# Kernel optimization log

Measured on AMD Instinct MI355X. Metric: run time of the kernel, lower is better.

The kernel has to match this reference:

```python
import jax, jax.numpy as jnp
import numpy as np

B, T, C, H = 2, 2048, 1024, 16
D = C // H  # head dim


def setup_inputs() -> dict:
    key = jax.random.key(0)
    k1, k2, k3 = jax.random.split(key, 3)
    x = jax.random.normal(k1, (B, T, C), dtype=jnp.float32)
    w_qkv = jax.random.normal(k2, (3 * C, C), dtype=jnp.float32) * (1.0 / np.sqrt(C))
    b_qkv = jnp.zeros((3 * C,), dtype=jnp.float32)
    w_proj = jax.random.normal(k3, (C, C), dtype=jnp.float32) * (1.0 / np.sqrt(C))
    b_proj = jnp.zeros((C,), dtype=jnp.float32)
    return {"x": x, "w_qkv": w_qkv, "b_qkv": b_qkv, "w_proj": w_proj, "b_proj": b_proj}


def reference(x, w_qkv, b_qkv, w_proj, b_proj):
    # torch Linear: y = x @ W^T + b
    qkv = jnp.einsum('btc,oc->bto', x, w_qkv) + b_qkv  # [B,T,3C]
    q, k, v = jnp.split(qkv, 3, axis=-1)
    # [B,T,C] -> [B,H,T,D]
    reshape = lambda t: t.reshape(B, T, H, D).transpose(0, 2, 1, 3)
    q, k, v = reshape(q), reshape(k), reshape(v)
    scale = 1.0 / jnp.sqrt(jnp.float32(C))  # NOTE: full C, as in source
    att = jnp.einsum('bhtd,bhsd->bhts', q, k) * scale  # [B,H,T,T]
    causal = jnp.tril(jnp.ones((T, T), dtype=bool))
    att = jnp.where(causal, att, -jnp.inf)
    att = jax.nn.softmax(att, axis=-1)
    y = jnp.einsum('bhts,bhsd->bhtd', att, v)  # [B,H,T,D]
    y = y.transpose(0, 2, 1, 3).reshape(B, T, C)
    return jnp.einsum('btc,oc->bto', y, w_proj) + b_proj
```

## Files before the change

### kernel.cpp

```cpp
#include <hip/hip_runtime.h>

#define DEVINL __device__ __forceinline__

typedef __attribute__((ext_vector_type(8))) short short8;
typedef __attribute__((ext_vector_type(4))) float f32x4;

DEVINL unsigned f2bf_u(float x) {
  union { float f; unsigned u; } v; v.f = x;
  unsigned r = v.u + 0x7FFF + ((v.u >> 16) & 1);
  return r >> 16;
}
DEVINL unsigned short f2bf(float x) { return (unsigned short)f2bf_u(x); }

DEVINL unsigned cvt_pk_bf16(float lo, float hi) {
  unsigned r;
  asm("v_cvt_pk_bf16_f32 %0, %1, %2" : "=v"(r) : "v"(lo), "v"(hi));
  return r;
}

DEVINL void permlane32_swap(unsigned& a, unsigned& b) {
  asm volatile("v_permlane32_swap_b32 %0, %1" : "+v"(a), "+v"(b));
}
DEVINL void permlane16_swap(unsigned& a, unsigned& b) {
  asm volatile("v_permlane16_swap_b32 %0, %1" : "+v"(a), "+v"(b));
}

#if __has_builtin(__builtin_amdgcn_exp2f)
#define EXP2(x) __builtin_amdgcn_exp2f(x)
#else
#define EXP2(x) exp2f(x)
#endif

DEVINL void gload_lds16(const void* g, void* l) {
  __builtin_amdgcn_global_load_lds(
      (const __attribute__((address_space(1))) unsigned int*)g,
      (__attribute__((address_space(3))) unsigned int*)l, 16, 0, 0);
}

DEVINL short8 as_s8(uint4 v) { union { uint4 u; short8 s; } c; c.u = v; return c.s; }
DEVINL f32x4 fzero() { f32x4 z = {0.f, 0.f, 0.f, 0.f}; return z; }

__global__ __launch_bounds__(256) void cvt3_kernel(
    const float4* __restrict__ x, const float4* __restrict__ wq,
    const float4* __restrict__ wp, ushort4* __restrict__ xo,
    ushort4* __restrict__ wqo, ushort4* __restrict__ wpo) {
  const int N1 = 1048576, N2 = 1835008, NT = 2097152;
  int i = blockIdx.x * blockDim.x + threadIdx.x;
  int stride = gridDim.x * blockDim.x;
  for (; i < NT; i += stride) {
    const float4* s; ushort4* d; int j;
    if (i < N1) { s = x; d = xo; j = i; }
    else if (i < N2) { s = wq; d = wqo; j = i - N1; }
    else { s = wp; d = wpo; j = i - N2; }
    float4 v = s[j];
    ushort4 o;
    o.x = f2bf(v.x); o.y = f2bf(v.y); o.z = f2bf(v.z); o.w = f2bf(v.w);
    d[j] = o;
  }
}

template <int RX, int RY>
__global__ __launch_bounds__(256, 3) void gemm_qkv(
    const ushort* __restrict__ A, const ushort* __restrict__ Bw,
    const float* __restrict__ bias,
    ushort* __restrict__ Qb, ushort* __restrict__ Kb, ushort* __restrict__ Vt,
    int M, int N, int K) {
  __shared__ __align__(16) char smem[32768];
  char* ldsA = smem;
  char* ldsB = smem + 16384;

  int gx = gridDim.x;
  int id = blockIdx.y * gx + blockIdx.x;
  int xcd = id & 7, slot = id >> 3;
  int rw = gx / RX, rh = gridDim.y / RY;
  int bx = (xcd % RX) * rw + slot % rw;
  int by = (xcd / RX) * rh + slot / rw;

  int m0 = by * 128, n0 = bx * 128;
  int t = threadIdx.x;
  int lane = t & 63, w = t >> 6;
  int q = lane & 15, g = lane >> 4;
  int wr = w >> 1, wc = w & 1;

  int Lrow[4], Lcol[4];
#pragma unroll
  for (int i = 0; i < 4; ++i) {
    int L = i * 4096 + t * 16;
    int row = L >> 7, c = L & 127;
    Lrow[i] = row;
    Lcol[i] = c ^ ((row & 7) << 4);
  }
  const char* Abase = (const char*)A + (size_t)m0 * K * 2;
  const char* Bbase = (const char*)Bw + (size_t)n0 * K * 2;

  f32x4 acc[4][4];
#pragma unroll
  for (int i = 0; i < 4; ++i)
#pragma unroll
    for (int j = 0; j < 4; ++j) acc[i][j] = fzero();

  for (int k0 = 0; k0 < K; k0 += 64) {
    __syncthreads();
#pragma unroll
    for (int i = 0; i < 4; ++i) {
      int L = i * 4096 + t * 16;
      gload_lds16(Abase + (size_t)Lrow[i] * (K * 2) + k0 * 2 + Lcol[i], ldsA + L);
    }
#pragma unroll
    for (int i = 0; i < 4; ++i) {
      int L = i * 4096 + t * 16;
      gload_lds16(Bbase + (size_t)Lrow[i] * (K * 2) + k0 * 2 + Lcol[i], ldsB + L);
    }
    __syncthreads();

    uint4 bf[2][4];
#pragma unroll
    for (int s = 0; s < 2; ++s)
#pragma unroll
      for (int nt = 0; nt < 4; ++nt) {
        int row = wc * 64 + nt * 16 + q;
        int addr = row * 128 + ((g * 16 + 64 * s) ^ ((row & 7) << 4));
        bf[s][nt] = *(const uint4*)(ldsB + addr);
      }
#pragma unroll
    for (int mt = 0; mt < 4; ++mt) {
      int row = wr * 64 + mt * 16 + q;
      int a0 = row * 128 + ((g * 16) ^ ((row & 7) << 4));
      int a1 = row * 128 + ((g * 16 + 64) ^ ((row & 7) << 4));
      uint4 af0 = *(const uint4*)(ldsA + a0);
      uint4 af1 = *(const uint4*)(ldsA + a1);
#pragma unroll
      for (int nt = 0; nt < 4; ++nt) {
        acc[mt][nt] = __builtin_amdgcn_mfma_f32_16x16x32_bf16(
            as_s8(af0), as_s8(bf[0][nt]), acc[mt][nt], 0, 0, 0);
        acc[mt][nt] = __builtin_amdgcn_mfma_f32_16x16x32_bf16(
            as_s8(af1), as_s8(bf[1][nt]), acc[mt][nt], 0, 0, 0);
      }
    }
  }

  int mrow0 = m0 + wr * 64;
  int b = mrow0 >> 11, tt0 = mrow0 & 2047;
  if (n0 >= 2048) {
    int hs = (n0 + wc * 64) >> 6;
    int h = hs & 15;
    ushort* vb = Vt + ((size_t)(b * 16 + h) * 64) * 2048;
#pragma unroll
    for (int nt = 0; nt < 4; ++nt) {
      int d = nt * 16 + q;
      float bv = bias[n0 + wc * 64 + nt * 16 + q];
#pragma unroll
      for (int mt = 0; mt < 4; ++mt) {
        uint2 o;
        o.x = cvt_pk_bf16(acc[mt][nt][0] + bv, acc[mt][nt][1] + bv);
        o.y = cvt_pk_bf16(acc[mt][nt][2] + bv, acc[mt][nt][3] + bv);
        *(uint2*)(vb + (size_t)d * 2048 + tt0 + mt * 16 + g * 4) = o;
      }
    }
  } else {
    __syncthreads();
    char* tile = smem + w * 8192;
    float bv[4];
#pragma unroll
    for (int nt = 0; nt < 4; ++nt) bv[nt] = bias[n0 + wc * 64 + nt * 16 + q];
#pragma unroll
    for (int mt = 0; mt < 4; ++mt)
#pragma unroll
      for (int nt = 0; nt < 4; ++nt)
#pragma unroll
        for (int r = 0; r < 4; ++r) {
          int row = mt * 16 + g * 4 + r;
          int bcol = ((nt * 16 + q) * 2) ^ ((row & 7) << 4);
          *(ushort*)(tile + row * 128 + bcol) = f2bf(acc[mt][nt][r] + bv[nt]);
        }
    int hs = (n0 + wc * 64) >> 6;
    int which = hs >> 4, h = hs & 15;
    ushort* dst = which == 0 ? Qb : Kb;
    ushort* dbase = dst + (size_t)(b * 16 + h) * 131072 + (size_t)tt0 * 64;
#pragma unroll
    for (int p = 0; p < 8; ++p) {
      int row = p * 8 + (lane >> 3);
      int bcol = ((lane & 7) * 16) ^ ((row & 7) << 4);
      uint4 v = *(const uint4*)(tile + row * 128 + bcol);
      *(uint4*)(dbase + (size_t)row * 64 + (lane & 7) * 8) = v;
    }
  }
}

__global__ __launch_bounds__(256, 2) void gemm_proj(
    const ushort* __restrict__ A, const ushort* __restrict__ Bw,
    const float* __restrict__ bias, float* __restrict__ Out,
    int M, int N, int K) {
  __shared__ __align__(16) char smem[24576];

  int gx = gridDim.x;
  int id = blockIdx.y * gx + blockIdx.x;
  int xcd = id & 7, slot = id >> 3;
  int bx = slot & 7;
  int by = xcd * 8 + (slot >> 3);

  int m0 = by * 64, n0 = bx * 128;
  int t = threadIdx.x;
  int lane = t & 63, w = t >> 6;
  int q = lane & 15, g = lane >> 4;
  int wr = w >> 1, wc = w & 1;

  int Lrow[4], Lcol[4];
#pragma unroll
  for (int i = 0; i < 4; ++i) {
    int L = i * 4096 + t * 16;
    int row = L >> 7, c = L & 127;
    Lrow[i] = row;
    Lcol[i] = c ^ ((row & 7) << 4);
  }
  const char* Abase = (const char*)A + (size_t)m0 * K * 2;
  const char* Bbase = (const char*)Bw + (size_t)n0 * K * 2;

  f32x4 acc[2][4];
#pragma unroll
  for (int i = 0; i < 2; ++i)
#pragma unroll
    for (int j = 0; j < 4; ++j) acc[i][j] = fzero();

  for (int k0 = 0; k0 < K; k0 += 64) {
    __syncthreads();
#pragma unroll
    for (int i = 0; i < 2; ++i) {
      int L = i * 4096 + t * 16;
      gload_lds16(Abase + (size_t)Lrow[i] * (K * 2) + k0 * 2 + Lcol[i], smem + L);
    }
#pragma unroll
    for (int i = 0; i < 4; ++i) {
      int L = i * 4096 + t * 16;
      gload_lds16(Bbase + (size_t)Lrow[i] * (K * 2) + k0 * 2 + Lcol[i],
                  smem + 8192 + L);
    }
    __syncthreads();

    uint4 bf[2][4];
#pragma unroll
    for (int s = 0; s < 2; ++s)
#pragma unroll
      for (int nt = 0; nt < 4; ++nt) {
        int row = wc * 64 + nt * 16 + q;
        int addr = 8192 + row * 128 + ((g * 16 + 64 * s) ^ ((row & 7) << 4));
        bf[s][nt] = *(const uint4*)(smem + addr);
      }
    __builtin_amdgcn_s_setprio(1);
#pragma unroll
    for (int mt = 0; mt < 2; ++mt) {
      int row = wr * 32 + mt * 16 + q;
      int a0 = row * 128 + ((g * 16) ^ ((row & 7) << 4));
      int a1 = row * 128 + ((g * 16 + 64) ^ ((row & 7) << 4));
      uint4 af0 = *(const uint4*)(smem + a0);
      uint4 af1 = *(const uint4*)(smem + a1);
#pragma unroll
      for (int nt = 0; nt < 4; ++nt) {
        acc[mt][nt] = __builtin_amdgcn_mfma_f32_16x16x32_bf16(
            as_s8(af0), as_s8(bf[0][nt]), acc[mt][nt], 0, 0, 0);
        acc[mt][nt] = __builtin_amdgcn_mfma_f32_16x16x32_bf16(
            as_s8(af1), as_s8(bf[1][nt]), acc[mt][nt], 0, 0, 0);
      }
    }
    __builtin_amdgcn_s_setprio(0);
  }

#pragma unroll
  for (int nt = 0; nt < 4; ++nt) {
    int ncol = n0 + wc * 64 + nt * 16 + q;
    float bv = bias[ncol];
#pragma unroll
    for (int mt = 0; mt < 2; ++mt)
#pragma unroll
      for (int r = 0; r < 4; ++r) {
        int m = m0 + wr * 32 + mt * 16 + g * 4 + r;
        Out[(size_t)m * N + ncol] = acc[mt][nt][r] + bv;
      }
  }
}

__global__ __launch_bounds__(512) void attn_kernel(
    const ushort* __restrict__ Q, const ushort* __restrict__ K,
    const ushort* __restrict__ Vt, ushort* __restrict__ Y) {
  __shared__ __align__(16) char smem[33280];
  const float C44 = 0.0450842298f;
  int id = blockIdx.x;
  int xcd = id & 7, slot = id >> 3;
  int bh = xcd * 4 + (slot & 3);
  int qt = 31 - (slot >> 2);
  int t = threadIdx.x;
  int lane = t & 63, w = t >> 6;
  int q = lane & 15, g = lane >> 4;
  int wq = w & 3, half = w >> 2;
  int b = bh >> 4, hh = bh & 15;

  const char* Kc0 = (const char*)(K + (size_t)bh * 2048 * 64);
  const char* Vc0 = (const char*)(Vt + (size_t)bh * 64 * 2048);

  int tb = t * 16;
  int srow = tb >> 7;
  int scol = (tb & 127) ^ ((srow & 7) << 4);

  int offK[2][2], offV[4];
#pragma unroll
  for (int sub = 0; sub < 2; ++sub)
#pragma unroll
    for (int s = 0; s < 2; ++s) {
      int row = half * 32 + sub * 16 + q;
      offK[sub][s] = row * 128 + ((g * 16 + 64 * s) ^ ((row & 7) << 4));
    }
#pragma unroll
  for (int ds = 0; ds < 4; ++ds) {
    int row = ds * 16 + q;
    offV[ds] = 8192 + row * 128 + ((half * 64 + g * 16) ^ ((row & 7) << 4));
  }

  int nch = qt + 1;
  int qrow0 = qt * 64 + wq * 16;
  int qg = qrow0 + q;

  uint4 qf[2];
  {
    const ushort* Qrow = Q + ((size_t)bh * 2048 + qrow0 + q) * 64;
    qf[0] = *(const uint4*)(Qrow + g * 8);
    qf[1] = *(const uint4*)(Qrow + 32 + g * 8);
  }

  f32x4 oacc[4];
#pragma unroll
  for (int i = 0; i < 4; ++i) oacc[i] = fzero();
  float l_run = 0.f;

  gload_lds16(Kc0 + (size_t)srow * 128 + scol, smem + tb);
  gload_lds16(Vc0 + (size_t)srow * 4096 + scol, smem + 8192 + tb);
  __syncthreads();

  int cur = 0;
#pragma unroll 1
  for (int c = 0; c < nch; ++c) {
    int kv0 = c * 64;
    if (c + 1 < nch) {
      int kn = kv0 + 64;
      char* dstb = smem + (cur ^ 1) * 16384;
      gload_lds16(Kc0 + (size_t)(kn + srow) * 128 + scol, dstb + tb);
      gload_lds16(Vc0 + (size_t)srow * 4096 + (size_t)kn * 2 + scol,
                  dstb + 8192 + tb);
    }
    const char* base = smem + cur * 16384;
    int kst = kv0 + half * 32;
    if (kst <= qrow0 + 15) {
      f32x4 sacc[2];
      __builtin_amdgcn_s_setprio(1);
#pragma unroll
      for (int sub = 0; sub < 2; ++sub) {
        sacc[sub] = fzero();
#pragma unroll
        for (int s = 0; s < 2; ++s)
          sacc[sub] = __builtin_amdgcn_mfma_f32_16x16x32_bf16(
              as_s8(*(const uint4*)(base + offK[sub][s])), as_s8(qf[s]),
              sacc[sub], 0, 0, 0);
      }
      __builtin_amdgcn_s_setprio(0);

      if (kst + 31 > qrow0) {
#pragma unroll
        for (int sub = 0; sub < 2; ++sub)
#pragma unroll
          for (int r = 0; r < 4; ++r) {
            int kv = kst + sub * 16 + g * 4 + r;
            if (kv > qg) sacc[sub][r] = -3e38f;
          }
      }

      unsigned pk[2][2];
      float psum = 0.f;
#pragma unroll
      for (int sub = 0; sub < 2; ++sub) {
        float p0 = EXP2(sacc[sub][0] * C44);
        float p1 = EXP2(sacc[sub][1] * C44);
        float p2 = EXP2(sacc[sub][2] * C44);
        float p3 = EXP2(sacc[sub][3] * C44);
        psum += (p0 + p1) + (p2 + p3);
        pk[sub][0] = cvt_pk_bf16(p0, p1);
        pk[sub][1] = cvt_pk_bf16(p2, p3);
      }
      l_run += psum;

      unsigned w0 = pk[0][0], w1 = pk[1][0];
      permlane32_swap(w0, w1);
      permlane16_swap(w0, w1);
      unsigned w2 = pk[0][1], w3 = pk[1][1];
      permlane32_swap(w2, w3);
      permlane16_swap(w2, w3);
      uint4 pa; pa.x = w0; pa.y = w2; pa.z = w1; pa.w = w3;

      __builtin_amdgcn_s_setprio(1);
#pragma unroll
      for (int ds = 0; ds < 4; ++ds)
        oacc[ds] = __builtin_amdgcn_mfma_f32_16x16x32_bf16(
            as_s8(pa), as_s8(*(const uint4*)(base + offV[ds])),
            oacc[ds], 0, 0, 0);
      __builtin_amdgcn_s_setprio(0);
    }

    __syncthreads();
    cur ^= 1;
  }

  l_run += __shfl_xor(l_run, 16);
  l_run += __shfl_xor(l_run, 32);
  float* ob = (float*)smem + wq * 1024;
  float* mlb = (float*)(smem + 32768);
  if (half) {
#pragma unroll
    for (int ds = 0; ds < 4; ++ds)
#pragma unroll
      for (int r = 0; r < 4; ++r)
        ob[(g * 4 + r) * 64 + ds * 16 + q] = oacc[ds][r];
    if (g == 0) mlb[wq * 16 + q] = l_run;
  }
  __syncthreads();
  if (!half) {
#pragma unroll
    for (int r = 0; r < 4; ++r) {
      int row = g * 4 + r;
      float lA = __shfl(l_run, row);
      float lB = mlb[wq * 16 + row];
      float linv = 1.0f / (lA + lB);
#pragma unroll
      for (int ds = 0; ds < 4; ++ds) {
        float vB = ob[row * 64 + ds * 16 + q];
        float yv = (oacc[ds][r] + vB) * linv;
        Y[(size_t)(b * 2048 + qrow0 + row) * 1024 + hh * 64 + ds * 16 + q] =
            f2bf(yv);
      }
    }
  }
}

extern "C" void kernel_launch(void* const* d_in, const int* in_sizes, int n_in,
                              void* d_out, int out_size, void* d_ws, size_t ws_size,
                              hipStream_t stream) {
  const float* x = (const float*)d_in[0];
  const float* w_qkv = (const float*)d_in[1];
  const float* b_qkv = (const float*)d_in[2];
  const float* w_proj = (const float*)d_in[3];
  const float* b_proj = (const float*)d_in[4];
  float* out = (float*)d_out;
  char* ws = (char*)d_ws;
  const size_t MB = 1024 * 1024;
  ushort* xb    = (ushort*)(ws + 0 * MB);
  ushort* wqkvb = (ushort*)(ws + 8 * MB);
  ushort* wprojb= (ushort*)(ws + 14 * MB);
  ushort* Qb    = (ushort*)(ws + 16 * MB);
  ushort* Kb    = (ushort*)(ws + 24 * MB);
  ushort* Vt    = (ushort*)(ws + 40 * MB);
  ushort* Yb    = (ushort*)(ws + 48 * MB);

  cvt3_kernel<<<2048, 256, 0, stream>>>((const float4*)x, (const float4*)w_qkv,
                                        (const float4*)w_proj, (ushort4*)xb,
                                        (ushort4*)wqkvb, (ushort4*)wprojb);
  gemm_qkv<2, 4><<<dim3(24, 32), 256, 0, stream>>>(xb, wqkvb, b_qkv, Qb, Kb, Vt,
                                                   4096, 3072, 1024);
  attn_kernel<<<dim3(1024), 512, 0, stream>>>(Qb, Kb, Vt, Yb);
  gemm_proj<<<dim3(8, 64), 256, 0, stream>>>(Yb, wprojb, b_proj, out, 4096,
                                             1024, 1024);
}
```

Before: 89.81 us.

## Split KV loop of long causal query tiles across two blocks with merge kernel

Query tiles 17–31 of each head are now handled by two blocks, each taking alternating KV chunks. Each block writes unnormalized fp32 partial outputs and row sums to workspace, and a new merge kernel adds the halves, normalizes and writes bf16 Y. Short tiles keep the single-block path. The goal is to shorten the critical path of the causal attention grid and balance work across CUs. The cost is an extra kernel launch, extra global traffic for the partials, and reuse of workspace regions that earlier stages wrote.

```diff
diff --git a/kernel.cpp b/kernel.cpp
--- a/kernel.cpp
+++ b/kernel.cpp
@@ -281,13 +281,17 @@
 
 __global__ __launch_bounds__(512) void attn_kernel(
     const ushort* __restrict__ Q, const ushort* __restrict__ K,
-    const ushort* __restrict__ Vt, ushort* __restrict__ Y) {
+    const ushort* __restrict__ Vt, ushort* __restrict__ Y,
+    float* __restrict__ Part, float* __restrict__ PartB) {
   __shared__ __align__(16) char smem[33280];
   const float C44 = 0.0450842298f;
   int id = blockIdx.x;
   int xcd = id & 7, slot = id >> 3;
-  int bh = xcd * 4 + (slot & 3);
-  int qt = 31 - (slot >> 2);
+  int h4 = slot & 3, j = slot >> 2;
+  int bh = xcd * 4 + h4;
+  int qt, p, c0, cstep; bool split;
+  if (j < 30) { split = true;  qt = 31 - (j >> 1); p = j & 1; c0 = p; cstep = 2; }
+  else        { split = false; qt = 46 - j;        p = 0;     c0 = 0; cstep = 1; }
   int t = threadIdx.x;
   int lane = t & 63, w = t >> 6;
   int q = lane & 15, g = lane >> 4;
@@ -315,7 +319,6 @@
     offV[ds] = 8192 + row * 128 + ((half * 64 + g * 16) ^ ((row & 7) << 4));
   }
 
-  int nch = qt + 1;
   int qrow0 = qt * 64 + wq * 16;
   int qg = qrow0 + q;
 
@@ -331,16 +334,20 @@
   for (int i = 0; i < 4; ++i) oacc[i] = fzero();
   float l_run = 0.f;
 
-  gload_lds16(Kc0 + (size_t)srow * 128 + scol, smem + tb);
-  gload_lds16(Vc0 + (size_t)srow * 4096 + scol, smem + 8192 + tb);
+  {
+    int kv00 = c0 * 64;
+    gload_lds16(Kc0 + (size_t)(kv00 + srow) * 128 + scol, smem + tb);
+    gload_lds16(Vc0 + (size_t)srow * 4096 + (size_t)kv00 * 2 + scol,
+                smem + 8192 + tb);
+  }
   __syncthreads();
 
   int cur = 0;
 #pragma unroll 1
-  for (int c = 0; c < nch; ++c) {
+  for (int c = c0; c <= qt; c += cstep) {
     int kv0 = c * 64;
-    if (c + 1 < nch) {
-      int kn = kv0 + 64;
+    if (c + cstep <= qt) {
+      int kn = (c + cstep) * 64;
       char* dstb = smem + (cur ^ 1) * 16384;
       gload_lds16(Kc0 + (size_t)(kn + srow) * 128 + scol, dstb + tb);
       gload_lds16(Vc0 + (size_t)srow * 4096 + (size_t)kn * 2 + scol,
@@ -421,20 +428,66 @@
   }
   __syncthreads();
   if (!half) {
-#pragma unroll
-    for (int r = 0; r < 4; ++r) {
-      int row = g * 4 + r;
-      float lA = __shfl(l_run, row);
-      float lB = mlb[wq * 16 + row];
-      float linv = 1.0f / (lA + lB);
-#pragma unroll
-      for (int ds = 0; ds < 4; ++ds) {
-        float vB = ob[row * 64 + ds * 16 + q];
-        float yv = (oacc[ds][r] + vB) * linv;
-        Y[(size_t)(b * 2048 + qrow0 + row) * 1024 + hh * 64 + ds * 16 + q] =
-            f2bf(yv);
-      }
-    }
+    if (!split) {
+#pragma unroll
+      for (int r = 0; r < 4; ++r) {
+        int row = g * 4 + r;
+        float lA = __shfl(l_run, row);
+        float lB = mlb[wq * 16 + row];
+        float linv = 1.0f / (lA + lB);
+#pragma unroll
+        for (int ds = 0; ds < 4; ++ds) {
+          float vB = ob[row * 64 + ds * 16 + q];
+          float yv = (oacc[ds][r] + vB) * linv;
+          Y[(size_t)(b * 2048 + qrow0 + row) * 1024 + hh * 64 + ds * 16 + q] =
+              f2bf(yv);
+        }
+      }
+    } else {
+      int pi = (bh * 15 + (qt - 17)) * 2 + p;
+      float* P = (pi < 840) ? Part + (size_t)pi * 4160
+                            : PartB + (size_t)(pi - 840) * 4160;
+#pragma unroll
+      for (int r = 0; r < 4; ++r) {
+        int row = g * 4 + r;
+        int gr = wq * 16 + row;
+        float lA = __shfl(l_run, row);
+        float lB = mlb[wq * 16 + row];
+        if (q == 0) P[4096 + gr] = lA + lB;
+#pragma unroll
+        for (int ds = 0; ds < 4; ++ds) {
+          float vB = ob[row * 64 + ds * 16 + q];
+          P[(size_t)gr * 64 + ds * 16 + q] = oacc[ds][r] + vB;
+        }
+      }
+    }
+  }
+}
+
+__global__ __launch_bounds__(256) void attn_merge(
+    const float* __restrict__ Part, const float* __restrict__ PartB,
+    ushort* __restrict__ Y) {
+  int m = blockIdx.x;
+  int bh = m / 15, ti = m % 15, qt = 17 + ti;
+  int pi0 = (bh * 15 + ti) * 2, pi1 = pi0 + 1;
+  const float* P0 = (pi0 < 840) ? Part + (size_t)pi0 * 4160
+                                : PartB + (size_t)(pi0 - 840) * 4160;
+  const float* P1 = (pi1 < 840) ? Part + (size_t)pi1 * 4160
+                                : PartB + (size_t)(pi1 - 840) * 4160;
+  int tid = threadIdx.x;
+  int e = tid * 16;
+  int row = e >> 6, col0 = e & 63;
+  float linv = 1.0f / (P0[4096 + row] + P1[4096 + row]);
+  int b = bh >> 4, hh = bh & 15;
+  ushort* y = Y + (size_t)(b * 2048 + qt * 64 + row) * 1024 + hh * 64 + col0;
+#pragma unroll
+  for (int i = 0; i < 16; i += 4) {
+    float4 a = *(const float4*)(P0 + e + i);
+    float4 c = *(const float4*)(P1 + e + i);
+    uint2 o;
+    o.x = cvt_pk_bf16((a.x + c.x) * linv, (a.y + c.y) * linv);
+    o.y = cvt_pk_bf16((a.z + c.z) * linv, (a.w + c.w) * linv);
+    *(uint2*)(y + i) = o;
   }
 }
 
@@ -454,15 +507,18 @@
   ushort* wprojb= (ushort*)(ws + 14 * MB);
   ushort* Qb    = (ushort*)(ws + 16 * MB);
   ushort* Kb    = (ushort*)(ws + 24 * MB);
+  float*  PartB = (float*)(ws + 32 * MB);
   ushort* Vt    = (ushort*)(ws + 40 * MB);
   ushort* Yb    = (ushort*)(ws + 48 * MB);
+  float*  Part  = (float*)(ws + 0 * MB);
 
   cvt3_kernel<<<2048, 256, 0, stream>>>((const float4*)x, (const float4*)w_qkv,
                                         (const float4*)w_proj, (ushort4*)xb,
                                         (ushort4*)wqkvb, (ushort4*)wprojb);
   gemm_qkv<2, 4><<<dim3(24, 32), 256, 0, stream>>>(xb, wqkvb, b_qkv, Qb, Kb, Vt,
                                                    4096, 3072, 1024);
-  attn_kernel<<<dim3(1024), 512, 0, stream>>>(Qb, Kb, Vt, Yb);
+  attn_kernel<<<dim3(1504), 512, 0, stream>>>(Qb, Kb, Vt, Yb, Part, PartB);
+  attn_merge<<<dim3(480), 256, 0, stream>>>(Part, PartB, Yb);
   gemm_proj<<<dim3(8, 64), 256, 0, stream>>>(Yb, wprojb, b_proj, out, 4096,
                                              1024, 1024);
 }
```

Result: slower. 97.14 us (+8.2%).
